# Kernel tuning notes

Hardware: AMD Instinct MI355X
Metric: run time of the kernel (lower is better)

The kernel has to match this reference:

```python
import jax, jax.numpy as jnp
import numpy as np

B, T, C = 4, 2048, 1024
H = 16
HD = C // H  # 64
OBS_DIM, ACT_DIM = 17, 6
JOINED_DIM = OBS_DIM + ACT_DIM + 2  # 25


def _make_mask():
    # tril causal mask with every (JOINED_DIM-1 + k*JOINED_DIM)-th column zeroed (RL branch)
    m = np.tril(np.ones((T, T), dtype=np.float32))
    m[:, JOINED_DIM - 1::JOINED_DIM] = 0.0
    return jnp.asarray(m > 0)  # bool [T, T]


MASK = _make_mask()


def setup_inputs() -> dict:
    key = jax.random.key(0)
    ks = jax.random.split(key, 9)
    s = 1.0 / np.sqrt(C)
    return {
        "x": jax.random.normal(ks[0], (B, T, C), dtype=jnp.float32),
        "Wq": jax.random.normal(ks[1], (C, C), dtype=jnp.float32) * s,
        "bq": jax.random.normal(ks[2], (C,), dtype=jnp.float32) * s,
        "Wk": jax.random.normal(ks[3], (C, C), dtype=jnp.float32) * s,
        "bk": jax.random.normal(ks[4], (C,), dtype=jnp.float32) * s,
        "Wv": jax.random.normal(ks[5], (C, C), dtype=jnp.float32) * s,
        "bv": jax.random.normal(ks[6], (C,), dtype=jnp.float32) * s,
        "Wp": jax.random.normal(ks[7], (C, C), dtype=jnp.float32) * s,
        "bp": jax.random.normal(ks[8], (C,), dtype=jnp.float32) * s,
    }


def reference(x, Wq, bq, Wk, bk, Wv, bv, Wp, bp):
    # torch nn.Linear: y = x @ W.T + b
    def split_heads(t):  # [B,T,C] -> [B,H,T,HD]
        return t.reshape(B, T, H, HD).transpose(0, 2, 1, 3)

    q = split_heads(x @ Wq.T + bq)
    k = split_heads(x @ Wk.T + bk)
    v = split_heads(x @ Wv.T + bv)

    att = jnp.einsum("bhqd,bhkd->bhqk", q, k) * (1.0 / np.sqrt(HD))
    att = jnp.where(MASK[None, None, :, :], att, -jnp.inf)
    att = jax.nn.softmax(att, axis=-1)
    # dropout layers are identity in eval mode

    y = jnp.einsum("bhqk,bhkd->bhqd", att, v)  # [B,H,T,HD]
    y = y.transpose(0, 2, 1, 3).reshape(B, T, C)
    return y @ Wp.T + bp
```

## Files before the change

### kernel.cpp

```cpp
#include <hip/hip_runtime.h>
#include <hip/hip_bf16.h>


typedef __attribute__((ext_vector_type(8))) short short8;
typedef __attribute__((ext_vector_type(4))) short short4v;
typedef __attribute__((ext_vector_type(4))) float floatx4;
typedef unsigned short us;

__device__ __forceinline__ us f2bf(float f){
    union { __hip_bfloat16 h; us u; } cv;
    cv.h = __float2bfloat16(f);
    return cv.u;
}

__device__ __forceinline__ void ld_g2l16(const void* g, void* l){
    __builtin_amdgcn_global_load_lds((const __attribute__((address_space(1))) void*)g,
                                     (__attribute__((address_space(3))) void*)l, 16, 0, 0);
}

__global__ __launch_bounds__(256) void cvt_kernel(const float* __restrict__ in,
                                                  us* __restrict__ out, int n4){
    int i = blockIdx.x * 256 + threadIdx.x;
    if (i < n4){
        float4 v = reinterpret_cast<const float4*>(in)[i];
        ushort4 o;
        o.x = f2bf(v.x); o.y = f2bf(v.y); o.z = f2bf(v.z); o.w = f2bf(v.w);
        reinterpret_cast<ushort4*>(out)[i] = o;
    }
}

__global__ __launch_bounds__(256) void cvt4_kernel(const float* __restrict__ w0, const float* __restrict__ w1,
                                                   const float* __restrict__ w2, const float* __restrict__ w3,
                                                   us* __restrict__ o0, us* __restrict__ o1,
                                                   us* __restrict__ o2, us* __restrict__ o3){
    int wsel = blockIdx.x >> 10;
    int i = (blockIdx.x & 1023) * 256 + threadIdx.x;
    const float* src = (wsel == 0) ? w0 : (wsel == 1) ? w1 : (wsel == 2) ? w2 : w3;
    us* dst = (wsel == 0) ? o0 : (wsel == 1) ? o1 : (wsel == 2) ? o2 : o3;
    float4 v = reinterpret_cast<const float4*>(src)[i];
    ushort4 o;
    o.x = f2bf(v.x); o.y = f2bf(v.y); o.z = f2bf(v.z); o.w = f2bf(v.w);
    reinterpret_cast<ushort4*>(dst)[i] = o;
}


#define QSCALE 0.1803368801111244f

#define BAR() __builtin_amdgcn_s_barrier()
#define LGKM0() do { asm volatile("s_waitcnt lgkmcnt(0)" ::: "memory"); __builtin_amdgcn_sched_barrier(0); } while(0)
#define VMC6() asm volatile("s_waitcnt vmcnt(6)" ::: "memory")
#define VMC0() asm volatile("s_waitcnt vmcnt(0)" ::: "memory")

#define STAGE_A3(buf, kt) do { \
    _Pragma("unroll") \
    for (int c_ = 0; c_ < 4; c_++) \
        ld_g2l16(Ag + (size_t)(m0 + srow[c_])*1024 + (kt)*64 + sgr[c_]*8, \
                 &smem[(buf)*24576 + (c_*8 + wave)*512]); \
} while(0)

#define STAGE_B3(buf, kt) do { \
    _Pragma("unroll") \
    for (int c_ = 0; c_ < 2; c_++) \
        ld_g2l16(Wb + (size_t)(n0 + srow[c_])*1024 + (kt)*64 + sgr[c_]*8, \
                 &smem[(buf)*24576 + 16384 + (c_*8 + wave)*512]); \
} while(0)

#define LOAD_F3(buf, KS) do { \
    _Pragma("unroll") \
    for (int i_ = 0; i_ < 4; i_++){ \
        int ra_ = wmm*64 + i_*16 + lane15; \
        int ga_ = ((KS)*4 + quad) ^ (ra_ & 7); \
        af[i_] = *reinterpret_cast<const short8*>(&smem[(buf)*24576 + ra_*64 + ga_*8]); \
    } \
    _Pragma("unroll") \
    for (int j_ = 0; j_ < 4; j_++){ \
        int rb_ = wnn*64 + j_*16 + lane15; \
        int gb_ = ((KS)*4 + quad) ^ (rb_ & 7); \
        bf[j_] = *reinterpret_cast<const short8*>(&smem[(buf)*24576 + 16384 + rb_*64 + gb_*8]); \
    } \
} while(0)

#define MFMA_KS() do { \
    __builtin_amdgcn_s_setprio(1); \
    _Pragma("unroll") \
    for (int i_ = 0; i_ < 4; i_++) \
        _Pragma("unroll") \
        for (int j_ = 0; j_ < 4; j_++) \
            acc[i_][j_] = __builtin_amdgcn_mfma_f32_16x16x32_bf16( \
                af[i_], bf[j_], acc[i_][j_], 0, 0, 0); \
    __builtin_amdgcn_s_setprio(0); \
} while(0)

__global__ __launch_bounds__(512, 2) void gemm_qkv3(
    const us* __restrict__ Ag,
    const us* __restrict__ Wqb, const us* __restrict__ Wkb, const us* __restrict__ Wvb,
    const float* __restrict__ bq, const float* __restrict__ bk, const float* __restrict__ bv,
    us* __restrict__ qo, us* __restrict__ ko, us* __restrict__ vto)
{
    __shared__ us smem[73728];
    const int tid = threadIdx.x;
    const int lane = tid & 63;
    const int wave = tid >> 6;
    const int lane15 = lane & 15;
    const int quad = lane >> 4;
    const int wmm = wave & 3;
    const int wnn = wave >> 2;
    const int seg = blockIdx.x >> 3;
    const int n0 = (blockIdx.x & 7) * 128;
    const int m0 = blockIdx.y * 256;

    const us* Wb = (seg == 0) ? Wqb : (seg == 1) ? Wkb : Wvb;
    const float* bias = (seg == 0) ? bq : (seg == 1) ? bk : bv;

    int srow[4], sgr[4];
    #pragma unroll
    for (int c = 0; c < 4; c++){
        int s = (c*8 + wave)*64 + lane;
        srow[c] = s >> 3;
        sgr[c] = (s & 7) ^ ((s >> 3) & 7);
    }

    floatx4 zero = {0.f, 0.f, 0.f, 0.f};
    floatx4 acc[4][4];
    #pragma unroll
    for (int i = 0; i < 4; i++)
        #pragma unroll
        for (int j = 0; j < 4; j++) acc[i][j] = zero;
    short8 af[4];
    short8 bf[4];

    STAGE_A3(0, 0); STAGE_B3(0, 0);
    STAGE_A3(1, 1); STAGE_B3(1, 1);
    VMC6(); BAR();

    #pragma unroll
    for (int t = 0; t < 16; t++){
        const int cur = t % 3, nxt = (t + 2) % 3;
        LOAD_F3(cur, 0);
        if (t < 14) STAGE_A3(nxt, t + 2);
        BAR(); LGKM0();
        MFMA_KS();
        BAR();
        LOAD_F3(cur, 1);
        if (t < 14) STAGE_B3(nxt, t + 2);
        BAR(); LGKM0();
        MFMA_KS();
        if (t < 14) { VMC6(); } else { VMC0(); }
        BAR();
    }

    if (seg < 2){
        #pragma unroll
        for (int i = 0; i < 4; i++){
            #pragma unroll
            for (int j = 0; j < 4; j++){
                int n = n0 + wnn*64 + j*16 + lane15;
                float bvv = bias[n];
                #pragma unroll
                for (int r = 0; r < 4; r++){
                    int m = m0 + wmm*64 + i*16 + quad*4 + r;
                    float val = acc[i][j][r] + bvv;
                    if (seg == 0){
                        qo[(size_t)m*1024 + n] = f2bf(val * QSCALE);
                    } else {
                        int b = m >> 11, tt = m & 2047;
                        int h = n >> 6,  d = n & 63;
                        ko[(((size_t)b*16 + h)*2048 + tt)*64 + d] = f2bf(val);
                    }
                }
            }
        }
    } else {
        us* lCT = smem;
        const int b = m0 >> 11;
        const int t0 = m0 & 2047;
        #pragma unroll
        for (int j = 0; j < 4; j++){
            int nl = wnn*64 + j*16 + lane15;
            float bvv = bias[n0 + nl];
            #pragma unroll
            for (int i = 0; i < 4; i++){
                int ml = wmm*64 + i*16 + quad*4;
                unsigned int lo = (unsigned int)f2bf(acc[i][j][0] + bvv) |
                                  ((unsigned int)f2bf(acc[i][j][1] + bvv) << 16);
                unsigned int hi = (unsigned int)f2bf(acc[i][j][2] + bvv) |
                                  ((unsigned int)f2bf(acc[i][j][3] + bvv) << 16);
                uint2 pk2; pk2.x = lo; pk2.y = hi;
                *reinterpret_cast<uint2*>(&lCT[(size_t)nl*264 + ml]) = pk2;
            }
        }
        __syncthreads();
        int nl = tid >> 2;
        int c4 = tid & 3;
        int nC = n0 + nl;
        int h = nC >> 6, d = nC & 63;
        us* dst = vto + (((size_t)b*16 + h)*64 + d)*2048 + t0 + c4*64;
        int rr = (t0 + c4*64) % 25;
        #pragma unroll
        for (int ii = 0; ii < 8; ii++){
            uint4 v = *reinterpret_cast<const uint4*>(&lCT[(size_t)nl*264 + c4*64 + ii*8]);
            us* pv = reinterpret_cast<us*>(&v);
            #pragma unroll
            for (int e = 0; e < 8; e++){
                if (rr == 24) pv[e] = 0;
                rr = (rr == 24) ? 0 : rr + 1;
            }
            *reinterpret_cast<uint4*>(dst + ii*8) = v;
        }
    }
}

__device__ __forceinline__ short8 rdP(const us* pw, int lane15, int ks, int quad){
    const us* a = &pw[lane15*68 + ks*32 + quad*8];
    short4v lo = *reinterpret_cast<const short4v*>(a);
    short4v hi = *reinterpret_cast<const short4v*>(a + 4);
    short8 r = {lo[0], lo[1], lo[2], lo[3], hi[0], hi[1], hi[2], hi[3]};
    return r;
}

__device__ __forceinline__ void pstore_plain(floatx4 (&s)[4], us* pw, int lane15, int quad){
    #pragma unroll
    for (int tj = 0; tj < 4; tj++)
        #pragma unroll
        for (int r = 0; r < 4; r++)
            pw[(quad*4 + r)*68 + tj*16 + lane15] = f2bf(__builtin_amdgcn_exp2f(s[tj][r]));
}

__device__ __forceinline__ void pstore_diag(floatx4 (&s)[4], us* pw, int rgrow, int j0,
                                            int lane15, int quad){
    #pragma unroll
    for (int tj = 0; tj < 4; tj++){
        #pragma unroll
        for (int r = 0; r < 4; r++){
            float p = __builtin_amdgcn_exp2f(s[tj][r]);
            bool kill = (j0 + tj*16 + lane15) > (rgrow + quad*4 + r);
            pw[(quad*4 + r)*68 + tj*16 + lane15] = f2bf(kill ? 0.f : p);
        }
    }
}

#define ATT_STAGE(itn) do { \
    _Pragma("unroll") \
    for (int i_ = 0; i_ < 2; i_++){ \
        ld_g2l16(kb + (size_t)((itn)*64 + srow[i_])*64 + sgr[i_]*8, &lK[(itn) & 1][(i_*4 + wave)*512]); \
        ld_g2l16(vb + (size_t)srow[i_]*2048 + (itn)*64 + sgr[i_]*8, &lV[(itn) & 1][(i_*4 + wave)*512]); \
    } } while(0)

#define ATT_BODY(MODE, ITV) do { \
    const int j0_ = (ITV)*64; \
    __syncthreads(); \
    if ((ITV) + 1 < nIter) ATT_STAGE((ITV) + 1); \
    const us* Kb = lK[(ITV) & 1]; \
    const us* Vb = lV[(ITV) & 1]; \
    floatx4 s0[4], s1[4]; \
    __builtin_amdgcn_s_setprio(1); \
    _Pragma("unroll") \
    for (int tj = 0; tj < 4; tj++){ \
        int rk = tj*16 + lane15; \
        short8 kf0 = *reinterpret_cast<const short8*>(&Kb[rk*64 + ((quad     ^ (rk & 7)))*8]); \
        short8 kf1 = *reinterpret_cast<const short8*>(&Kb[rk*64 + (((4+quad) ^ (rk & 7)))*8]); \
        floatx4 z1 = __builtin_amdgcn_mfma_f32_16x16x32_bf16(qf1a, kf0, zero, 0, 0, 0); \
        s1[tj]     = __builtin_amdgcn_mfma_f32_16x16x32_bf16(qf1b, kf1, z1,   0, 0, 0); \
        if ((MODE) != 2){ \
            floatx4 z0 = __builtin_amdgcn_mfma_f32_16x16x32_bf16(qf0a, kf0, zero, 0, 0, 0); \
            s0[tj]     = __builtin_amdgcn_mfma_f32_16x16x32_bf16(qf0b, kf1, z0,   0, 0, 0); \
        } \
    } \
    __builtin_amdgcn_s_setprio(0); \
    if ((MODE) == 2)      pstore_diag(s1, pw1, rg1, j0_, lane15, quad); \
    else                  pstore_plain(s1, pw1, lane15, quad); \
    if ((MODE) == 1)      pstore_diag(s0, pw0, rg0, j0_, lane15, quad); \
    else if ((MODE) == 0) pstore_plain(s0, pw0, lane15, quad); \
    __builtin_amdgcn_s_setprio(1); \
    _Pragma("unroll") \
    for (int ks = 0; ks < 2; ks++){ \
        short8 mfr = *reinterpret_cast<const short8*>(&lmask[j0_ + ks*32 + quad*8]); \
        short8 pf1 = rdP(pw1, lane15, ks, quad); \
        short8 pf0; \
        lacc1 = __builtin_amdgcn_mfma_f32_16x16x32_bf16(pf1, mfr, lacc1, 0, 0, 0); \
        if ((MODE) != 2){ \
            pf0 = rdP(pw0, lane15, ks, quad); \
            lacc0 = __builtin_amdgcn_mfma_f32_16x16x32_bf16(pf0, mfr, lacc0, 0, 0, 0); \
        } \
        _Pragma("unroll") \
        for (int dt = 0; dt < 4; dt++){ \
            int rv = dt*16 + lane15; \
            short8 vf = *reinterpret_cast<const short8*>(&Vb[rv*64 + (((ks*4+quad) ^ (rv & 7)))*8]); \
            acc1[dt] = __builtin_amdgcn_mfma_f32_16x16x32_bf16(pf1, vf, acc1[dt], 0, 0, 0); \
            if ((MODE) != 2) acc0[dt] = __builtin_amdgcn_mfma_f32_16x16x32_bf16(pf0, vf, acc0[dt], 0, 0, 0); \
        } \
    } \
    __builtin_amdgcn_s_setprio(0); \
} while(0)

__global__ __launch_bounds__(256, 3) void flash_attn(
    const us* __restrict__ q,
    const us* __restrict__ k,
    const us* __restrict__ vT,
    us* __restrict__ y)
{
    __shared__ us lK[2][64*64];
    __shared__ us lV[2][64*64];
    __shared__ us lP[4][2][16*68];
    __shared__ us lmask[2048];
    const int tid = threadIdx.x;
    const int lane = tid & 63;
    const int wave = tid >> 6;
    const int lane15 = lane & 15;
    const int quad = lane >> 4;
    const int lin = blockIdx.x;
    const int qt2 = 15 - (lin >> 6);
    const int bh = lin & 63;
    const int b = bh >> 4, h = bh & 15;
    const int rg0 = qt2*128 + wave*16;
    const int rg1 = rg0 + 64;
    const int nIter = 2*qt2 + 2;

    const us* kb = k  + (size_t)bh*2048*64;
    const us* vb = vT + (size_t)bh*64*2048;

    {
        int c0 = tid * 8;
        int rr = c0 % 25;
        ushort4 mv[2];
        us* pm = reinterpret_cast<us*>(mv);
        #pragma unroll
        for (int e = 0; e < 8; e++){
            pm[e] = (rr == 24) ? (us)0 : (us)0x3F80;
            rr = (rr == 24) ? 0 : rr + 1;
        }
        *reinterpret_cast<uint4*>(&lmask[c0]) = *reinterpret_cast<uint4*>(mv);
    }

    floatx4 zero = {0.f, 0.f, 0.f, 0.f};
    us* pw0 = &lP[wave][0][0];
    us* pw1 = &lP[wave][1][0];

    int srow[2], sgr[2];
    #pragma unroll
    for (int i = 0; i < 2; i++){
        int s = (i*4 + wave)*64 + lane;
        srow[i] = s >> 3;
        sgr[i] = (s & 7) ^ ((s >> 3) & 7);
    }

    const us* q0 = q + ((size_t)b*2048 + rg0 + lane15)*1024 + h*64 + quad*8;
    const us* q1 = q + ((size_t)b*2048 + rg1 + lane15)*1024 + h*64 + quad*8;
    short8 qf0a = *reinterpret_cast<const short8*>(q0);
    short8 qf0b = *reinterpret_cast<const short8*>(q0 + 32);
    short8 qf1a = *reinterpret_cast<const short8*>(q1);
    short8 qf1b = *reinterpret_cast<const short8*>(q1 + 32);

    floatx4 acc0[4], acc1[4];
    #pragma unroll
    for (int d = 0; d < 4; d++){ acc0[d] = zero; acc1[d] = zero; }
    floatx4 lacc0 = zero, lacc1 = zero;

    ATT_STAGE(0);

    int it = 0;
    #pragma unroll 1
    for (; it < nIter - 2; it++) ATT_BODY(0, it);
    ATT_BODY(1, it); it++;
    ATT_BODY(2, it);

    float rl0[4], rl1[4];
    #pragma unroll
    for (int r = 0; r < 4; r++){ rl0[r] = 1.0f / lacc0[r]; rl1[r] = 1.0f / lacc1[r]; }
    #pragma unroll
    for (int dt = 0; dt < 4; dt++){
        #pragma unroll
        for (int r = 0; r < 4; r++){
            int t0 = rg0 + quad*4 + r;
            int t1 = rg1 + quad*4 + r;
            int cc = h*64 + dt*16 + lane15;
            y[((size_t)b*2048 + t0)*1024 + cc] = f2bf(acc0[dt][r] * rl0[r]);
            y[((size_t)b*2048 + t1)*1024 + cc] = f2bf(acc1[dt][r] * rl1[r]);
        }
    }
}

__global__ __launch_bounds__(512, 2) void gemm_out3(
    const us* __restrict__ Ag,
    const us* __restrict__ Wb,
    const float* __restrict__ bias,
    float* __restrict__ out)
{
    __shared__ us smem[73728];
    const int tid = threadIdx.x;
    const int lane = tid & 63;
    const int wave = tid >> 6;
    const int lane15 = lane & 15;
    const int quad = lane >> 4;
    const int wmm = wave & 3;
    const int wnn = wave >> 2;
    const int n0 = blockIdx.x * 128;
    const int m0 = blockIdx.y * 256;

    int srow[4], sgr[4];
    #pragma unroll
    for (int c = 0; c < 4; c++){
        int s = (c*8 + wave)*64 + lane;
        srow[c] = s >> 3;
        sgr[c] = (s & 7) ^ ((s >> 3) & 7);
    }

    floatx4 zero = {0.f, 0.f, 0.f, 0.f};
    floatx4 acc[4][4];
    #pragma unroll
    for (int i = 0; i < 4; i++)
        #pragma unroll
        for (int j = 0; j < 4; j++) acc[i][j] = zero;
    short8 af[4];
    short8 bf[4];

    STAGE_A3(0, 0); STAGE_B3(0, 0);
    STAGE_A3(1, 1); STAGE_B3(1, 1);
    VMC6(); BAR();

    #pragma unroll
    for (int t = 0; t < 16; t++){
        const int cur = t % 3, nxt = (t + 2) % 3;
        LOAD_F3(cur, 0);
        if (t < 14) STAGE_A3(nxt, t + 2);
        BAR(); LGKM0();
        MFMA_KS();
        BAR();
        LOAD_F3(cur, 1);
        if (t < 14) STAGE_B3(nxt, t + 2);
        BAR(); LGKM0();
        MFMA_KS();
        if (t < 14) { VMC6(); } else { VMC0(); }
        BAR();
    }

    #pragma unroll
    for (int i = 0; i < 4; i++){
        #pragma unroll
        for (int j = 0; j < 4; j++){
            int n = n0 + wnn*64 + j*16 + lane15;
            float bvv = bias[n];
            #pragma unroll
            for (int r = 0; r < 4; r++){
                int m = m0 + wmm*64 + i*16 + quad*4 + r;
                out[(size_t)m*1024 + n] = acc[i][j][r] + bvv;
            }
        }
    }
}

extern "C" void kernel_launch(void* const* d_in, const int* in_sizes, int n_in,
                              void* d_out, int out_size, void* d_ws, size_t ws_size,
                              hipStream_t stream)
{
    const float* x  = (const float*)d_in[0];
    const float* Wq = (const float*)d_in[1];
    const float* bq = (const float*)d_in[2];
    const float* Wk = (const float*)d_in[3];
    const float* bk = (const float*)d_in[4];
    const float* Wv = (const float*)d_in[5];
    const float* bv = (const float*)d_in[6];
    const float* Wp = (const float*)d_in[7];
    const float* bp = (const float*)d_in[8];
    float* out = (float*)d_out;

    us* ws  = (us*)d_ws;
    us* xbf = ws;
    us* wqb = xbf + (size_t)8192*1024;
    us* wkb = wqb + (size_t)1024*1024;
    us* wvb = wkb + (size_t)1024*1024;
    us* wpb = wvb + (size_t)1024*1024;
    us* qws = wpb + (size_t)1024*1024;
    us* kws = qws + (size_t)8388608;
    us* vtw = kws + (size_t)8388608;
    us* yws = vtw + (size_t)8388608;

    cvt_kernel<<<8192, 256, 0, stream>>>(x, xbf, 2097152);
    cvt4_kernel<<<4096, 256, 0, stream>>>(Wq, Wk, Wv, Wp, wqb, wkb, wvb, wpb);

    gemm_qkv3<<<dim3(24, 32), 512, 0, stream>>>(xbf, wqb, wkb, wvb, bq, bk, bv, qws, kws, vtw);

    flash_attn<<<1024, 256, 0, stream>>>(qws, kws, vtw, yws);

    gemm_out3<<<dim3(8, 32), 512, 0, stream>>>(yws, wpb, bp, out);
}
```

Baseline: 258.5 us.

## Double-buffer MFMA fragments to overlap LDS reads with matrix math in GEMMs

Restructures the K-loop of the QKV and output-projection GEMMs so that two sets of register fragments alternate. The LDS reads for the next half-step are issued before the MFMAs of the current half-step, and the per-iteration barriers are reduced. This is meant to hide LDS read latency behind MFMA work and cut barrier stalls. The cost is more VGPRs for the second fragment set, which may pressure occupancy under launch_bounds(512,2), and the vmcnt wait thresholds are changed.

```diff
diff --git a/kernel.cpp b/kernel.cpp
--- a/kernel.cpp
+++ b/kernel.cpp
@@ -47,8 +47,10 @@
 #define QSCALE 0.1803368801111244f
 
 #define BAR() __builtin_amdgcn_s_barrier()
+#define SGB0() __builtin_amdgcn_sched_barrier(0)
 #define LGKM0() do { asm volatile("s_waitcnt lgkmcnt(0)" ::: "memory"); __builtin_amdgcn_sched_barrier(0); } while(0)
 #define VMC6() asm volatile("s_waitcnt vmcnt(6)" ::: "memory")
+#define VMC4() asm volatile("s_waitcnt vmcnt(4)" ::: "memory")
 #define VMC0() asm volatile("s_waitcnt vmcnt(0)" ::: "memory")
 
 #define STAGE_A3(buf, kt) do { \
@@ -65,30 +67,55 @@
                  &smem[(buf)*24576 + 16384 + (c_*8 + wave)*512]); \
 } while(0)
 
-#define LOAD_F3(buf, KS) do { \
+#define LOAD_SET3(buf, KS, AF, BF) do { \
     _Pragma("unroll") \
     for (int i_ = 0; i_ < 4; i_++){ \
         int ra_ = wmm*64 + i_*16 + lane15; \
         int ga_ = ((KS)*4 + quad) ^ (ra_ & 7); \
-        af[i_] = *reinterpret_cast<const short8*>(&smem[(buf)*24576 + ra_*64 + ga_*8]); \
+        AF[i_] = *reinterpret_cast<const short8*>(&smem[(buf)*24576 + ra_*64 + ga_*8]); \
     } \
     _Pragma("unroll") \
     for (int j_ = 0; j_ < 4; j_++){ \
         int rb_ = wnn*64 + j_*16 + lane15; \
         int gb_ = ((KS)*4 + quad) ^ (rb_ & 7); \
-        bf[j_] = *reinterpret_cast<const short8*>(&smem[(buf)*24576 + 16384 + rb_*64 + gb_*8]); \
+        BF[j_] = *reinterpret_cast<const short8*>(&smem[(buf)*24576 + 16384 + rb_*64 + gb_*8]); \
     } \
 } while(0)
 
-#define MFMA_KS() do { \
+#define MFMA_SET3(AF, BF) do { \
     __builtin_amdgcn_s_setprio(1); \
     _Pragma("unroll") \
     for (int i_ = 0; i_ < 4; i_++) \
         _Pragma("unroll") \
         for (int j_ = 0; j_ < 4; j_++) \
             acc[i_][j_] = __builtin_amdgcn_mfma_f32_16x16x32_bf16( \
-                af[i_], bf[j_], acc[i_][j_], 0, 0, 0); \
+                AF[i_], BF[j_], acc[i_][j_], 0, 0, 0); \
     __builtin_amdgcn_s_setprio(0); \
+} while(0)
+
+#define KLOOP3() do { \
+    STAGE_A3(0, 0); STAGE_B3(0, 0); \
+    STAGE_A3(1, 1); STAGE_B3(1, 1); \
+    VMC6(); BAR(); \
+    LOAD_SET3(0, 0, afE, bfE); LGKM0(); \
+    _Pragma("unroll") \
+    for (int t = 0; t < 16; t++){ \
+        const int cur = t % 3, nxt = (t + 2) % 3, nx1 = (t + 1) % 3; \
+         \
+        LOAD_SET3(cur, 1, afO, bfO); \
+        SGB0(); \
+        if (t < 14) STAGE_A3(nxt, t + 2); \
+        MFMA_SET3(afE, bfE); \
+        LGKM0(); \
+        if (t < 14) { VMC4(); } else if (t == 14) { VMC0(); } \
+        BAR(); \
+         \
+        if (t < 15){ LOAD_SET3(nx1, 0, afE, bfE); SGB0(); } \
+        if (t < 14) STAGE_B3(nxt, t + 2); \
+        MFMA_SET3(afO, bfO); \
+        LGKM0(); \
+        BAR(); \
+    } \
 } while(0)
 
 __global__ __launch_bounds__(512, 2) void gemm_qkv3(
@@ -126,28 +153,9 @@
     for (int i = 0; i < 4; i++)
         #pragma unroll
         for (int j = 0; j < 4; j++) acc[i][j] = zero;
-    short8 af[4];
-    short8 bf[4];
-
-    STAGE_A3(0, 0); STAGE_B3(0, 0);
-    STAGE_A3(1, 1); STAGE_B3(1, 1);
-    VMC6(); BAR();
-
-    #pragma unroll
-    for (int t = 0; t < 16; t++){
-        const int cur = t % 3, nxt = (t + 2) % 3;
-        LOAD_F3(cur, 0);
-        if (t < 14) STAGE_A3(nxt, t + 2);
-        BAR(); LGKM0();
-        MFMA_KS();
-        BAR();
-        LOAD_F3(cur, 1);
-        if (t < 14) STAGE_B3(nxt, t + 2);
-        BAR(); LGKM0();
-        MFMA_KS();
-        if (t < 14) { VMC6(); } else { VMC0(); }
-        BAR();
-    }
+    short8 afE[4], bfE[4], afO[4], bfO[4];
+
+    KLOOP3();
 
     if (seg < 2){
         #pragma unroll
@@ -411,28 +419,9 @@
     for (int i = 0; i < 4; i++)
         #pragma unroll
         for (int j = 0; j < 4; j++) acc[i][j] = zero;
-    short8 af[4];
-    short8 bf[4];
-
-    STAGE_A3(0, 0); STAGE_B3(0, 0);
-    STAGE_A3(1, 1); STAGE_B3(1, 1);
-    VMC6(); BAR();
-
-    #pragma unroll
-    for (int t = 0; t < 16; t++){
-        const int cur = t % 3, nxt = (t + 2) % 3;
-        LOAD_F3(cur, 0);
-        if (t < 14) STAGE_A3(nxt, t + 2);
-        BAR(); LGKM0();
-        MFMA_KS();
-        BAR();
-        LOAD_F3(cur, 1);
-        if (t < 14) STAGE_B3(nxt, t + 2);
-        BAR(); LGKM0();
-        MFMA_KS();
-        if (t < 14) { VMC6(); } else { VMC0(); }
-        BAR();
-    }
+    short8 afE[4], bfE[4], afO[4], bfO[4];
+
+    KLOOP3();
 
     #pragma unroll
     for (int i = 0; i < 4; i++){
```

Measured after the change: 256.4 us. Within noise of the previous version (-0.8%).
